# Kernel tuning notes

Hardware: AMD Instinct MI355X
Metric: run time of the kernel (lower is better)

The kernel has to match this reference:

```python
import jax, jax.numpy as jnp
import numpy as np

B, L, SIZE, ATT, LIN = 8, 2048, 1024, 1024, 4096
EPS = 1e-5


def layer_norm(x, g, b):
    m = x.mean(-1, keepdims=True)
    v = ((x - m) ** 2).mean(-1, keepdims=True)
    return (x - m) * jax.lax.rsqrt(v + EPS) * g + b


def time_shift(x):
    # ZeroPad2d((0,0,1,-1)): prepend a zero timestep, drop the last one
    return jnp.pad(x, ((0, 0), (1, 0), (0, 0)))[:, :-1]


def wkv(time_decay, time_first, k, v):
    """RWKV-v4 WKV linear-attention recurrence (numerically stable, log-space max tracking).
    k, v: (B, L, D). Returns (B, L, D)."""
    w = -jnp.exp(time_decay)  # (D,) per-channel decay (negative)
    u = time_first            # (D,) bonus for current token

    def step(carry, kv):
        p, q, o = carry  # numerator, denominator, running max exponent: (B, D)
        kt, vt = kv      # (B, D)
        no = jnp.maximum(o, u + kt)
        A = jnp.exp(o - no)
        Bc = jnp.exp(u + kt - no)
        out = (A * p + Bc * vt) / (A * q + Bc)
        no2 = jnp.maximum(o + w, kt)
        A2 = jnp.exp(o + w - no2)
        B2 = jnp.exp(kt - no2)
        return (A2 * p + B2 * vt, A2 * q + B2, no2), out

    Bn, Ln, D = k.shape
    init = (jnp.zeros((Bn, D), k.dtype), jnp.zeros((Bn, D), k.dtype),
            jnp.full((Bn, D), -1e38, k.dtype))
    _, out = jax.lax.scan(step, init, (jnp.moveaxis(k, 1, 0), jnp.moveaxis(v, 1, 0)))
    return jnp.moveaxis(out, 0, 1)


def setup_inputs() -> dict:
    key = jax.random.key(0)
    ks = jax.random.split(key, 20)
    n = lambda i, shape, s=1.0: jax.random.normal(ks[i], shape, jnp.float32) * s
    u = lambda i, shape: jax.random.uniform(ks[i], shape, jnp.float32)
    return {
        "x": n(0, (B, L, SIZE)),
        "ln_att_g": jnp.ones((SIZE,), jnp.float32), "ln_att_b": jnp.zeros((SIZE,), jnp.float32),
        "ln_ffn_g": jnp.ones((SIZE,), jnp.float32), "ln_ffn_b": jnp.zeros((SIZE,), jnp.float32),
        "att_time_decay": n(1, (ATT,), 0.5), "att_time_first": n(2, (ATT,), 0.5),
        "att_mix_k": u(3, (SIZE,)), "att_mix_v": u(4, (SIZE,)), "att_mix_r": u(5, (SIZE,)),
        "att_wk": n(6, (SIZE, ATT), 0.02), "att_wv": n(7, (SIZE, ATT), 0.02),
        "att_wr": n(8, (SIZE, ATT), 0.02), "att_wo": n(9, (ATT, SIZE), 0.02),
        "ffn_mix_k": u(10, (SIZE,)), "ffn_mix_r": u(11, (SIZE,)),
        "ffn_wk": n(12, (SIZE, LIN), 0.02), "ffn_wv": n(13, (LIN, SIZE), 0.02),
        "ffn_wr": n(14, (SIZE, SIZE), 0.02),
    }


def reference(x, ln_att_g, ln_att_b, ln_ffn_g, ln_ffn_b,
              att_time_decay, att_time_first, att_mix_k, att_mix_v, att_mix_r,
              att_wk, att_wv, att_wr, att_wo,
              ffn_mix_k, ffn_mix_r, ffn_wk, ffn_wv, ffn_wr):
    # --- time-mixing (WKV attention) branch ---
    h = layer_norm(x, ln_att_g, ln_att_b)
    sx = time_shift(h)
    k = (h * att_mix_k + sx * (1.0 - att_mix_k)) @ att_wk
    v = (h * att_mix_v + sx * (1.0 - att_mix_v)) @ att_wv
    r = jax.nn.sigmoid((h * att_mix_r + sx * (1.0 - att_mix_r)) @ att_wr)
    att = (r * wkv(att_time_decay, att_time_first, k, v)) @ att_wo
    x = x + att  # dropout rate 0.0 (eval)
    # --- channel-mixing (FFN) branch ---
    h = layer_norm(x, ln_ffn_g, ln_ffn_b)
    sx = time_shift(h)
    kf = jnp.square(jax.nn.relu((h * ffn_mix_k + sx * (1.0 - ffn_mix_k)) @ ffn_wk))
    rf = jax.nn.sigmoid((h * ffn_mix_r + sx * (1.0 - ffn_mix_r)) @ ffn_wr)
    return x + rf * (kf @ ffn_wv)
```

## Files before the change

### kernel.cpp

```cpp
#include <hip/hip_runtime.h>
#include <cstdint>
#include <cstddef>

#define BB   8
#define LLEN 2048
#define DSZ  1024
#define FFN  4096
#define MROWS (BB*LLEN)
#define EPSLN 1e-5f
#define WKV_C 32
#define WKV_S (LLEN/WKV_C)
#define WKV_STATES (BB*WKV_C*DSZ)

typedef __bf16 bh8 __attribute__((ext_vector_type(8)));
typedef float  f32x4 __attribute__((ext_vector_type(4)));

__device__ __forceinline__ unsigned short f32_to_bf16(float f) {
  unsigned int u = __float_as_uint(f);
  u += 0x7FFFu + ((u >> 16) & 1u);
  return (unsigned short)(u >> 16);
}
__device__ __forceinline__ float bf16_to_f32(unsigned short u) {
  return __uint_as_float(((unsigned int)u) << 16);
}
__device__ __forceinline__ float bf16_lo(unsigned int u) {
  return __uint_as_float(u << 16);
}
__device__ __forceinline__ float bf16_hi(unsigned int u) {
  return __uint_as_float(u & 0xFFFF0000u);
}
__device__ __forceinline__ unsigned int pack_bf16(float lo, float hi) {
  return (unsigned int)f32_to_bf16(lo) | ((unsigned int)f32_to_bf16(hi) << 16);
}

__device__ __forceinline__ void load_lds16(const void* g, void* l) {
  __builtin_amdgcn_global_load_lds((const __attribute__((address_space(1))) void*)g,
                                   (__attribute__((address_space(3))) void*)l, 16, 0, 0);
}

#define RAW_BAR() asm volatile("s_barrier" ::: "memory")
#define WAIT_VM6() asm volatile("s_waitcnt vmcnt(6)" ::: "memory")
#define WAIT_VM0() asm volatile("s_waitcnt vmcnt(0)" ::: "memory")

__global__ __launch_bounds__(256) void transpose_bf16(const float* __restrict__ W,
                                                      unsigned short* __restrict__ Wt,
                                                      int K, int N) {
  __shared__ float tile[32][33];
  int n0 = blockIdx.x * 32, k0 = blockIdx.y * 32;
  int tx = threadIdx.x, ty = threadIdx.y;
#pragma unroll
  for (int j = 0; j < 32; j += 8)
    tile[ty + j][tx] = W[(size_t)(k0 + ty + j) * N + n0 + tx];
  __syncthreads();
#pragma unroll
  for (int j = 0; j < 32; j += 8)
    Wt[(size_t)(n0 + ty + j) * K + k0 + tx] = f32_to_bf16(tile[tx][ty + j]);
}

__global__ __launch_bounds__(256) void lnmix_att(const float* __restrict__ x,
                                                 const float* __restrict__ g,
                                                 const float* __restrict__ bb,
                                                 const float* __restrict__ mk,
                                                 const float* __restrict__ mv,
                                                 const float* __restrict__ mr,
                                                 unsigned short* __restrict__ xk,
                                                 unsigned short* __restrict__ xv,
                                                 unsigned short* __restrict__ xr) {
  int row = blockIdx.x;
  int t = row & (LLEN - 1);
  int tid = threadIdx.x;
  float4 vc = ((const float4*)(x + (size_t)row * DSZ))[tid];
  float4 vp = make_float4(0.f, 0.f, 0.f, 0.f);
  if (t > 0) vp = ((const float4*)(x + (size_t)(row - 1) * DSZ))[tid];
  float sc = vc.x + vc.y + vc.z + vc.w;
  float qc = vc.x * vc.x + vc.y * vc.y + vc.z * vc.z + vc.w * vc.w;
  float sp = vp.x + vp.y + vp.z + vp.w;
  float qp = vp.x * vp.x + vp.y * vp.y + vp.z * vp.z + vp.w * vp.w;
#pragma unroll
  for (int off = 32; off; off >>= 1) {
    sc += __shfl_down(sc, off); qc += __shfl_down(qc, off);
    sp += __shfl_down(sp, off); qp += __shfl_down(qp, off);
  }
  __shared__ float red[16];
  int lane = tid & 63, w = tid >> 6;
  if (lane == 0) { red[w] = sc; red[4 + w] = qc; red[8 + w] = sp; red[12 + w] = qp; }
  __syncthreads();
  if (tid < 4) red[tid * 4] = red[tid * 4] + red[tid * 4 + 1] + red[tid * 4 + 2] + red[tid * 4 + 3];
  __syncthreads();
  const float invD = 1.f / DSZ;
  float mc = red[0] * invD, rc = rsqrtf(red[4] * invD - mc * mc + EPSLN);
  float mp = red[8] * invD, rp = rsqrtf(red[12] * invD - mp * mp + EPSLN);
  float4 G = ((const float4*)g)[tid], Bv = ((const float4*)bb)[tid];
  float c[4] = { vc.x, vc.y, vc.z, vc.w };
  float p[4] = { vp.x, vp.y, vp.z, vp.w };
  float Ga[4] = { G.x, G.y, G.z, G.w };
  float Ba[4] = { Bv.x, Bv.y, Bv.z, Bv.w };
  float4 K = ((const float4*)mk)[tid];
  float4 V = ((const float4*)mv)[tid];
  float4 R = ((const float4*)mr)[tid];
  float Ka[4] = { K.x, K.y, K.z, K.w };
  float Va[4] = { V.x, V.y, V.z, V.w };
  float Ra[4] = { R.x, R.y, R.z, R.w };
  ushort4 ok, ov, orr;
  unsigned short* okp = &ok.x; unsigned short* ovp = &ov.x; unsigned short* orp = &orr.x;
#pragma unroll
  for (int e = 0; e < 4; ++e) {
    float hc = (c[e] - mc) * rc * Ga[e] + Ba[e];
    float hp = (t > 0) ? (p[e] - mp) * rp * Ga[e] + Ba[e] : 0.f;
    okp[e] = f32_to_bf16(hc * Ka[e] + hp * (1.f - Ka[e]));
    ovp[e] = f32_to_bf16(hc * Va[e] + hp * (1.f - Va[e]));
    orp[e] = f32_to_bf16(hc * Ra[e] + hp * (1.f - Ra[e]));
  }
  size_t e4 = (size_t)row * DSZ + tid * 4;
  *(ushort4*)(xk + e4) = ok;
  *(ushort4*)(xv + e4) = ov;
  *(ushort4*)(xr + e4) = orr;
}

__global__ __launch_bounds__(256) void lnmix_ffn(const float* __restrict__ x,
                                                 const float* __restrict__ g,
                                                 const float* __restrict__ bb,
                                                 const float* __restrict__ mk,
                                                 const float* __restrict__ mr,
                                                 unsigned short* __restrict__ xk,
                                                 unsigned short* __restrict__ xr) {
  int row = blockIdx.x;
  int t = row & (LLEN - 1);
  int tid = threadIdx.x;
  float4 vc = ((const float4*)(x + (size_t)row * DSZ))[tid];
  float4 vp = make_float4(0.f, 0.f, 0.f, 0.f);
  if (t > 0) vp = ((const float4*)(x + (size_t)(row - 1) * DSZ))[tid];
  float sc = vc.x + vc.y + vc.z + vc.w;
  float qc = vc.x * vc.x + vc.y * vc.y + vc.z * vc.z + vc.w * vc.w;
  float sp = vp.x + vp.y + vp.z + vp.w;
  float qp = vp.x * vp.x + vp.y * vp.y + vp.z * vp.z + vp.w * vp.w;
#pragma unroll
  for (int off = 32; off; off >>= 1) {
    sc += __shfl_down(sc, off); qc += __shfl_down(qc, off);
    sp += __shfl_down(sp, off); qp += __shfl_down(qp, off);
  }
  __shared__ float red[16];
  int lane = tid & 63, w = tid >> 6;
  if (lane == 0) { red[w] = sc; red[4 + w] = qc; red[8 + w] = sp; red[12 + w] = qp; }
  __syncthreads();
  if (tid < 4) red[tid * 4] = red[tid * 4] + red[tid * 4 + 1] + red[tid * 4 + 2] + red[tid * 4 + 3];
  __syncthreads();
  const float invD = 1.f / DSZ;
  float mc = red[0] * invD, rc = rsqrtf(red[4] * invD - mc * mc + EPSLN);
  float mp = red[8] * invD, rp = rsqrtf(red[12] * invD - mp * mp + EPSLN);
  float4 G = ((const float4*)g)[tid], Bv = ((const float4*)bb)[tid];
  float c[4] = { vc.x, vc.y, vc.z, vc.w };
  float p[4] = { vp.x, vp.y, vp.z, vp.w };
  float Ga[4] = { G.x, G.y, G.z, G.w };
  float Ba[4] = { Bv.x, Bv.y, Bv.z, Bv.w };
  float4 K = ((const float4*)mk)[tid];
  float4 R = ((const float4*)mr)[tid];
  float Ka[4] = { K.x, K.y, K.z, K.w };
  float Ra[4] = { R.x, R.y, R.z, R.w };
  ushort4 ok, orr;
  unsigned short* okp = &ok.x; unsigned short* orp = &orr.x;
#pragma unroll
  for (int e = 0; e < 4; ++e) {
    float hc = (c[e] - mc) * rc * Ga[e] + Ba[e];
    float hp = (t > 0) ? (p[e] - mp) * rp * Ga[e] + Ba[e] : 0.f;
    okp[e] = f32_to_bf16(hc * Ka[e] + hp * (1.f - Ka[e]));
    orp[e] = f32_to_bf16(hc * Ra[e] + hp * (1.f - Ra[e]));
  }
  size_t e4 = (size_t)row * DSZ + tid * 4;
  *(ushort4*)(xk + e4) = ok;
  *(ushort4*)(xr + e4) = orr;
}

__global__ __launch_bounds__(256) void wkv_pass1(const unsigned int* __restrict__ kk2,
                                                 const unsigned int* __restrict__ vv2,
                                                 const float* __restrict__ td,
                                                 float* __restrict__ sP,
                                                 float* __restrict__ sQ,
                                                 float* __restrict__ sO) {
  int gid = blockIdx.x * 256 + threadIdx.x;
  int d2 = gid & 511;
  int bc = gid >> 9;
  int c  = bc & (WKV_C - 1);
  int b  = bc >> 5;
  int d0 = d2 * 2;
  float w0 = -expf(td[d0]), w1 = -expf(td[d0 + 1]);
  size_t base = ((size_t)b * LLEN + (size_t)c * WKV_S) * 512 + d2;
  float p0 = 0.f, q0 = 0.f, o0 = -1e38f;
  float p1 = 0.f, q1 = 0.f, o1 = -1e38f;
  unsigned int kc = kk2[base], vc = vv2[base];
  unsigned int kA = 0, vA = 0, kB = 0, vB = 0;
  if (WKV_S > 1) { kA = kk2[base + 512]; vA = vv2[base + 512]; }
  for (int t = 0; t < WKV_S; ++t) {
    if (t + 2 < WKV_S) {
      size_t nxt = base + (size_t)(t + 2) * 512;
      kB = kk2[nxt]; vB = vv2[nxt];
    } else { kB = 0; vB = 0; }
    {
      float kt = bf16_lo(kc), vt = bf16_lo(vc);
      float ow = o0 + w0;
      float no2 = fmaxf(ow, kt);
      float A2 = expf(ow - no2), B2 = expf(kt - no2);
      p0 = A2 * p0 + B2 * vt; q0 = A2 * q0 + B2; o0 = no2;
    }
    {
      float kt = bf16_hi(kc), vt = bf16_hi(vc);
      float ow = o1 + w1;
      float no2 = fmaxf(ow, kt);
      float A2 = expf(ow - no2), B2 = expf(kt - no2);
      p1 = A2 * p1 + B2 * vt; q1 = A2 * q1 + B2; o1 = no2;
    }
    kc = kA; vc = vA; kA = kB; vA = vB;
  }
  int sidx = (bc << 10) + d0;
  sP[sidx] = p0; sP[sidx + 1] = p1;
  sQ[sidx] = q0; sQ[sidx + 1] = q1;
  sO[sidx] = o0; sO[sidx + 1] = o1;
}

__global__ __launch_bounds__(256) void wkv_combine(const float* __restrict__ sP,
                                                   const float* __restrict__ sQ,
                                                   const float* __restrict__ sO,
                                                   const float* __restrict__ td,
                                                   float* __restrict__ pP,
                                                   float* __restrict__ pQ,
                                                   float* __restrict__ pO) {
  int gid = blockIdx.x * 256 + threadIdx.x;
  int d = gid & (DSZ - 1);
  int b = gid >> 10;
  float w = -expf(td[d]);
  float Sw = (float)WKV_S * w;
  float p = 0.f, q = 0.f, o = -1e38f;
  for (int c = 0; c < WKV_C; ++c) {
    size_t idx = (((size_t)b * WKV_C + c) << 10) + d;
    pP[idx] = p; pQ[idx] = q; pO[idx] = o;
    float lp = sP[idx], lq = sQ[idx], lo = sO[idx];
    float oin = o + Sw;
    float no  = fmaxf(oin, lo);
    float Ai  = expf(oin - no);
    float Al  = expf(lo - no);
    p = Ai * p + Al * lp;
    q = Ai * q + Al * lq;
    o = no;
  }
}

__global__ __launch_bounds__(256) void wkv_pass3(const unsigned int* __restrict__ kk2,
                                                 const unsigned int* __restrict__ vv2,
                                                 const unsigned int* __restrict__ rr2,
                                                 const float* __restrict__ td,
                                                 const float* __restrict__ tf,
                                                 const float* __restrict__ pP,
                                                 const float* __restrict__ pQ,
                                                 const float* __restrict__ pO,
                                                 unsigned int* __restrict__ rw2) {
  int gid = blockIdx.x * 256 + threadIdx.x;
  int d2 = gid & 511;
  int bc = gid >> 9;
  int c  = bc & (WKV_C - 1);
  int b  = bc >> 5;
  int d0 = d2 * 2;
  float w0 = -expf(td[d0]), w1 = -expf(td[d0 + 1]);
  float u0 = tf[d0], u1 = tf[d0 + 1];
  int sidx = (bc << 10) + d0;
  float p0 = pP[sidx], q0 = pQ[sidx], o0 = pO[sidx];
  float p1 = pP[sidx + 1], q1 = pQ[sidx + 1], o1 = pO[sidx + 1];
  size_t base = ((size_t)b * LLEN + (size_t)c * WKV_S) * 512 + d2;
  unsigned int kc = kk2[base], vc = vv2[base], rc = rr2[base];
  unsigned int kA = 0, vA = 0, rA = 0, kB = 0, vB = 0, rB = 0;
  if (WKV_S > 1) { kA = kk2[base + 512]; vA = vv2[base + 512]; rA = rr2[base + 512]; }
  for (int t = 0; t < WKV_S; ++t) {
    if (t + 2 < WKV_S) {
      size_t nxt = base + (size_t)(t + 2) * 512;
      kB = kk2[nxt]; vB = vv2[nxt]; rB = rr2[nxt];
    } else { kB = 0; vB = 0; rB = 0; }
    float out0, out1;
    {
      float kt = bf16_lo(kc), vt = bf16_lo(vc);
      float uk = u0 + kt;
      float no = fmaxf(o0, uk);
      float A  = expf(o0 - no), Bc = expf(uk - no);
      out0 = (A * p0 + Bc * vt) / (A * q0 + Bc);
      float ow = o0 + w0;
      float no2 = fmaxf(ow, kt);
      float A2 = expf(ow - no2), B2 = expf(kt - no2);
      p0 = A2 * p0 + B2 * vt; q0 = A2 * q0 + B2; o0 = no2;
    }
    {
      float kt = bf16_hi(kc), vt = bf16_hi(vc);
      float uk = u1 + kt;
      float no = fmaxf(o1, uk);
      float A  = expf(o1 - no), Bc = expf(uk - no);
      out1 = (A * p1 + Bc * vt) / (A * q1 + Bc);
      float ow = o1 + w1;
      float no2 = fmaxf(ow, kt);
      float A2 = expf(ow - no2), B2 = expf(kt - no2);
      p1 = A2 * p1 + B2 * vt; q1 = A2 * q1 + B2; o1 = no2;
    }
    rw2[base + (size_t)t * 512] = pack_bf16(bf16_lo(rc) * out0, bf16_hi(rc) * out1);
    kc = kA; vc = vA; rc = rA; kA = kB; vA = vB; rA = rB;
  }
}


__device__ __forceinline__ void stage_half(const unsigned short* __restrict__ gsrc,
                                           int Kd, unsigned char* lds_base,
                                           int lane, int wid) {
  int gcol = (((lane & 7) ^ (lane >> 3)) << 3);
  int grow = lane >> 3;
#pragma unroll
  for (int j = 0; j < 2; ++j) {
    int win = wid * 2 + j;
    const unsigned short* src = gsrc + (size_t)(win * 8 + grow) * Kd + gcol;
    load_lds16(src, lds_base + win * 1024 + lane * 16);
  }
}

template <int EPI>
__global__ __launch_bounds__(512, 2) void gemm256(const unsigned short* __restrict__ A,
                                                  const unsigned short* __restrict__ Bt,
                                                  float* __restrict__ C,
                                                  unsigned short* __restrict__ Cbf,
                                                  const float* __restrict__ aux1,
                                                  const unsigned short* __restrict__ aux2b,
                                                  int M, int N, int K) {
  extern __shared__ unsigned char sm[];
  unsigned char* smA = sm;
  unsigned char* smB = sm + 65536;

  const int tid  = threadIdx.x;
  const int lane = tid & 63;
  const int wid  = tid >> 6;
  const int wr   = wid >> 2;
  const int wc   = wid & 3;

  int nwg = gridDim.x;
  int gx  = N >> 8;
  int wg  = blockIdx.x;
  int swzid = ((nwg & 7) == 0) ? ((wg & 7) * (nwg >> 3) + (wg >> 3)) : wg;
  int bn = swzid % gx, bm = swzid / gx;

  const unsigned short* Ab = A  + (size_t)bm * 256 * K;
  const unsigned short* Bb = Bt + (size_t)bn * 256 * K;

  const int nk = K >> 6;

  const int r15 = lane & 15;
  const int sw0 = ((((lane >> 4)    ) ^ (lane & 7)) << 4);
  const int sw1 = (((4 | (lane >> 4)) ^ (lane & 7)) << 4);
  const int aRow = wr * 16384 + r15 * 128;
  const int bRow = wc * 8192  + r15 * 128;

  f32x4 acc[8][4];
#pragma unroll
  for (int i = 0; i < 8; ++i)
#pragma unroll
    for (int j = 0; j < 4; ++j)
#pragma unroll
      for (int e = 0; e < 4; ++e) acc[i][j][e] = 0.f;

  stage_half(Ab,                 K, smA,                 lane, wid);
  stage_half(Ab + (size_t)128*K, K, smA + 16384,         lane, wid);
  stage_half(Bb,                 K, smB,                 lane, wid);
  stage_half(Bb + (size_t)128*K, K, smB + 16384,         lane, wid);
  if (nk > 1) {
    stage_half(Bb + 64,                 K, smB + 32768,         lane, wid);
    stage_half(Ab + 64,                 K, smA + 32768,         lane, wid);
    stage_half(Ab + (size_t)128*K + 64, K, smA + 32768 + 16384, lane, wid);
    WAIT_VM6();
  } else {
    WAIT_VM0();
  }
  RAW_BAR();

  bh8 a03[4][2], a47[4][2], b01[2][2], b23[2][2];

  for (int t = 0; t < nk; ++t) {
    const int buf  = (t & 1) * 32768;
    const int bufn = buf ^ 32768;
    const int kb1  = (t + 1) << 6;
    const int kb2  = (t + 2) << 6;

#pragma unroll
    for (int mi = 0; mi < 4; ++mi) {
      a03[mi][0] = *(const bh8*)(smA + buf + aRow + mi * 2048 + sw0);
      a03[mi][1] = *(const bh8*)(smA + buf + aRow + mi * 2048 + sw1);
    }
#pragma unroll
    for (int nj = 0; nj < 2; ++nj) {
      b01[nj][0] = *(const bh8*)(smB + buf + bRow + nj * 2048 + sw0);
      b01[nj][1] = *(const bh8*)(smB + buf + bRow + nj * 2048 + sw1);
    }
    if (t + 1 < nk)
      stage_half(Bb + (size_t)128*K + kb1, K, smB + bufn + 16384, lane, wid);
    RAW_BAR();
    __builtin_amdgcn_s_setprio(1);
#pragma unroll
    for (int mi = 0; mi < 4; ++mi)
#pragma unroll
      for (int nj = 0; nj < 2; ++nj) {
        acc[mi][nj] = __builtin_amdgcn_mfma_f32_16x16x32_bf16(a03[mi][0], b01[nj][0], acc[mi][nj], 0, 0, 0);
        acc[mi][nj] = __builtin_amdgcn_mfma_f32_16x16x32_bf16(a03[mi][1], b01[nj][1], acc[mi][nj], 0, 0, 0);
      }
    __builtin_amdgcn_s_setprio(0);
    RAW_BAR();

#pragma unroll
    for (int nj = 0; nj < 2; ++nj) {
      b23[nj][0] = *(const bh8*)(smB + buf + bRow + (nj + 2) * 2048 + sw0);
      b23[nj][1] = *(const bh8*)(smB + buf + bRow + (nj + 2) * 2048 + sw1);
    }
    RAW_BAR();
    __builtin_amdgcn_s_setprio(1);
#pragma unroll
    for (int mi = 0; mi < 4; ++mi)
#pragma unroll
      for (int nj = 0; nj < 2; ++nj) {
        acc[mi][nj + 2] = __builtin_amdgcn_mfma_f32_16x16x32_bf16(a03[mi][0], b23[nj][0], acc[mi][nj + 2], 0, 0, 0);
        acc[mi][nj + 2] = __builtin_amdgcn_mfma_f32_16x16x32_bf16(a03[mi][1], b23[nj][1], acc[mi][nj + 2], 0, 0, 0);
      }
    __builtin_amdgcn_s_setprio(0);
    RAW_BAR();

#pragma unroll
    for (int mi = 0; mi < 4; ++mi) {
      a47[mi][0] = *(const bh8*)(smA + buf + aRow + (mi + 4) * 2048 + sw0);
      a47[mi][1] = *(const bh8*)(smA + buf + aRow + (mi + 4) * 2048 + sw1);
    }
    if (t + 2 < nk) stage_half(Bb + kb2, K, smB + buf, lane, wid);
    RAW_BAR();
    __builtin_amdgcn_s_setprio(1);
#pragma unroll
    for (int mi = 0; mi < 4; ++mi)
#pragma unroll
      for (int nj = 0; nj < 2; ++nj) {
        acc[mi + 4][nj] = __builtin_amdgcn_mfma_f32_16x16x32_bf16(a47[mi][0], b01[nj][0], acc[mi + 4][nj], 0, 0, 0);
        acc[mi + 4][nj] = __builtin_amdgcn_mfma_f32_16x16x32_bf16(a47[mi][1], b01[nj][1], acc[mi + 4][nj], 0, 0, 0);
      }
    __builtin_amdgcn_s_setprio(0);
    RAW_BAR();

    if (t + 2 < nk) {
      stage_half(Ab + kb2,                 K, smA + buf,         lane, wid);
      stage_half(Ab + (size_t)128*K + kb2, K, smA + buf + 16384, lane, wid);
    }
    RAW_BAR();
    __builtin_amdgcn_s_setprio(1);
#pragma unroll
    for (int mi = 0; mi < 4; ++mi)
#pragma unroll
      for (int nj = 0; nj < 2; ++nj) {
        acc[mi + 4][nj + 2] = __builtin_amdgcn_mfma_f32_16x16x32_bf16(a47[mi][0], b23[nj][0], acc[mi + 4][nj + 2], 0, 0, 0);
        acc[mi + 4][nj + 2] = __builtin_amdgcn_mfma_f32_16x16x32_bf16(a47[mi][1], b23[nj][1], acc[mi + 4][nj + 2], 0, 0, 0);
      }
    __builtin_amdgcn_s_setprio(0);
    if (t + 2 < nk) { WAIT_VM6(); } else { WAIT_VM0(); }
    RAW_BAR();
  }

  const int r4 = (lane >> 4) * 4, cn = lane & 15;
#pragma unroll
  for (int mi = 0; mi < 8; ++mi) {
#pragma unroll
    for (int nj = 0; nj < 4; ++nj) {
      int col = bn * 256 + wc * 64 + nj * 16 + cn;
#pragma unroll
      for (int e = 0; e < 4; ++e) {
        int row = bm * 256 + wr * 128 + mi * 16 + r4 + e;
        size_t idx = (size_t)row * N + col;
        float val = acc[mi][nj][e];
        if (EPI == 0) {
          Cbf[idx] = f32_to_bf16(val);
        } else if (EPI == 1) {
          Cbf[idx] = f32_to_bf16(1.f / (1.f + expf(-val)));
        } else if (EPI == 2) {
          C[idx] = aux1[idx] + val;
        } else if (EPI == 3) {
          float tt = val > 0.f ? val : 0.f;
          Cbf[idx] = f32_to_bf16(tt * tt);
        } else {
          C[idx] = aux1[idx] + bf16_to_f32(aux2b[idx]) * val;
        }
      }
    }
  }
}

extern "C" void kernel_launch(void* const* d_in, const int* in_sizes, int n_in,
                              void* d_out, int out_size, void* d_ws, size_t ws_size,
                              hipStream_t stream) {
  const float* x        = (const float*)d_in[0];
  const float* ln_att_g = (const float*)d_in[1];
  const float* ln_att_b = (const float*)d_in[2];
  const float* ln_ffn_g = (const float*)d_in[3];
  const float* ln_ffn_b = (const float*)d_in[4];
  const float* td       = (const float*)d_in[5];
  const float* tf       = (const float*)d_in[6];
  const float* amk      = (const float*)d_in[7];
  const float* amv      = (const float*)d_in[8];
  const float* amr      = (const float*)d_in[9];
  const float* att_wk   = (const float*)d_in[10];
  const float* att_wv   = (const float*)d_in[11];
  const float* att_wr   = (const float*)d_in[12];
  const float* att_wo   = (const float*)d_in[13];
  const float* fmk      = (const float*)d_in[14];
  const float* fmr      = (const float*)d_in[15];
  const float* ffn_wk   = (const float*)d_in[16];
  const float* ffn_wv   = (const float*)d_in[17];
  const float* ffn_wr   = (const float*)d_in[18];
  float* out = (float*)d_out;
  (void)in_sizes; (void)n_in; (void)out_size;

  const size_t WBYTES  = 4 * ((size_t)DSZ * DSZ * 2)
                       + (size_t)FFN * DSZ * 2
                       + (size_t)DSZ * FFN * 2
                       + (size_t)DSZ * DSZ * 2;
  const size_t BUF     = (size_t)MROWS * DSZ * 2;
  const size_t NEEDED  = WBYTES + 4 * BUF + 2 * BUF;
  if (ws_size < NEEDED) return;

  char* ws = (char*)d_ws;
  size_t off = 0;
  auto take = [&](size_t bytes) { char* p = ws + off; off += (bytes + 255) & ~(size_t)255; return p; };

  unsigned short* wkT  = (unsigned short*)take((size_t)DSZ * DSZ * 2);
  unsigned short* wvT  = (unsigned short*)take((size_t)DSZ * DSZ * 2);
  unsigned short* wrT  = (unsigned short*)take((size_t)DSZ * DSZ * 2);
  unsigned short* woT  = (unsigned short*)take((size_t)DSZ * DSZ * 2);
  unsigned short* fwkT = (unsigned short*)take((size_t)FFN * DSZ * 2);
  unsigned short* fwvT = (unsigned short*)take((size_t)DSZ * FFN * 2);
  unsigned short* fwrT = (unsigned short*)take((size_t)DSZ * DSZ * 2);
  unsigned short* bufA = (unsigned short*)take(BUF);
  unsigned short* bufB = (unsigned short*)take(BUF);
  unsigned short* bufC = (unsigned short*)take(BUF);
  unsigned short* bufD = (unsigned short*)take(BUF);
  char*           eReg = take(2 * BUF);
  unsigned short* kf = bufC;

  float* sP = (float*)eReg;
  float* sQ = sP + WKV_STATES;
  float* sO = sQ + WKV_STATES;
  float* pP = sO + WKV_STATES;
  float* pQ = pP + WKV_STATES;
  float* pO = pQ + WKV_STATES;

  dim3 tb(32, 8);
  transpose_bf16<<<dim3(DSZ / 32, DSZ / 32), tb, 0, stream>>>(att_wk, wkT, DSZ, DSZ);
  transpose_bf16<<<dim3(DSZ / 32, DSZ / 32), tb, 0, stream>>>(att_wv, wvT, DSZ, DSZ);
  transpose_bf16<<<dim3(DSZ / 32, DSZ / 32), tb, 0, stream>>>(att_wr, wrT, DSZ, DSZ);
  transpose_bf16<<<dim3(DSZ / 32, DSZ / 32), tb, 0, stream>>>(att_wo, woT, DSZ, DSZ);
  transpose_bf16<<<dim3(FFN / 32, DSZ / 32), tb, 0, stream>>>(ffn_wk, fwkT, DSZ, FFN);
  transpose_bf16<<<dim3(DSZ / 32, FFN / 32), tb, 0, stream>>>(ffn_wv, fwvT, FFN, DSZ);
  transpose_bf16<<<dim3(DSZ / 32, DSZ / 32), tb, 0, stream>>>(ffn_wr, fwrT, DSZ, DSZ);

  const int LDSB = 131072;
  const int G1   = (MROWS / 256) * (DSZ / 256);
  const int G2   = (MROWS / 256) * (FFN / 256);

  lnmix_att<<<MROWS, 256, 0, stream>>>(x, ln_att_g, ln_att_b, amk, amv, amr, bufA, bufB, bufC);
  gemm256<0><<<G1, 512, LDSB, stream>>>(bufA, wkT, nullptr, bufD, nullptr, nullptr, MROWS, DSZ, DSZ);
  gemm256<0><<<G1, 512, LDSB, stream>>>(bufB, wvT, nullptr, bufA, nullptr, nullptr, MROWS, DSZ, DSZ);
  gemm256<1><<<G1, 512, LDSB, stream>>>(bufC, wrT, nullptr, bufB, nullptr, nullptr, MROWS, DSZ, DSZ);
  wkv_pass1<<<(WKV_STATES / 2) / 256, 256, 0, stream>>>((const unsigned int*)bufD, (const unsigned int*)bufA, td, sP, sQ, sO);
  wkv_combine<<<(BB * DSZ) / 256, 256, 0, stream>>>(sP, sQ, sO, td, pP, pQ, pO);
  wkv_pass3<<<(WKV_STATES / 2) / 256, 256, 0, stream>>>((const unsigned int*)bufD, (const unsigned int*)bufA, (const unsigned int*)bufB, td, tf, pP, pQ, pO, (unsigned int*)bufC);
  gemm256<2><<<G1, 512, LDSB, stream>>>(bufC, woT, out, nullptr, x, nullptr, MROWS, DSZ, DSZ);

  lnmix_ffn<<<MROWS, 256, 0, stream>>>(out, ln_ffn_g, ln_ffn_b, fmk, fmr, bufA, bufB);
  gemm256<3><<<G2, 512, LDSB, stream>>>(bufA, fwkT, nullptr, kf, nullptr, nullptr, MROWS, FFN, DSZ);
  gemm256<1><<<G1, 512, LDSB, stream>>>(bufB, fwrT, nullptr, bufA, nullptr, nullptr, MROWS, DSZ, DSZ);
  gemm256<4><<<G1, 512, LDSB, stream>>>(kf, fwvT, out, nullptr, out, bufA, MROWS, DSZ, FFN);
}
```

Before: 685.5 us.

## Replace 256x256 pipelined GEMM with simpler 128x256 tile, BK=32 double-buffered kernel

Swaps the hand-scheduled 256x256 GEMM (BK=64, staged quarter-loads, setprio, raw barriers) for a 128x256 tile kernel with BK=32, one-ahead double buffering and a single __syncthreads per k-step. LDS use drops from 128 KB to 48 KB and launch bounds allow 4 blocks per CU, aiming for more occupancy and simpler latency hiding. In exchange, each block does less reuse per byte loaded, runs fewer MFMAs between barriers, and loses the fine-grained interleaving of loads and compute.

```diff
diff --git a/kernel.cpp b/kernel.cpp
--- a/kernel.cpp
+++ b/kernel.cpp
@@ -37,10 +37,6 @@
   __builtin_amdgcn_global_load_lds((const __attribute__((address_space(1))) void*)g,
                                    (__attribute__((address_space(3))) void*)l, 16, 0, 0);
 }
-
-#define RAW_BAR() asm volatile("s_barrier" ::: "memory")
-#define WAIT_VM6() asm volatile("s_waitcnt vmcnt(6)" ::: "memory")
-#define WAIT_VM0() asm volatile("s_waitcnt vmcnt(0)" ::: "memory")
 
 __global__ __launch_bounds__(256) void transpose_bf16(const float* __restrict__ W,
                                                       unsigned short* __restrict__ Wt,
@@ -301,31 +297,17 @@
   }
 }
 
-
-__device__ __forceinline__ void stage_half(const unsigned short* __restrict__ gsrc,
-                                           int Kd, unsigned char* lds_base,
-                                           int lane, int wid) {
-  int gcol = (((lane & 7) ^ (lane >> 3)) << 3);
-  int grow = lane >> 3;
-#pragma unroll
-  for (int j = 0; j < 2; ++j) {
-    int win = wid * 2 + j;
-    const unsigned short* src = gsrc + (size_t)(win * 8 + grow) * Kd + gcol;
-    load_lds16(src, lds_base + win * 1024 + lane * 16);
-  }
-}
-
 template <int EPI>
-__global__ __launch_bounds__(512, 2) void gemm256(const unsigned short* __restrict__ A,
-                                                  const unsigned short* __restrict__ Bt,
-                                                  float* __restrict__ C,
-                                                  unsigned short* __restrict__ Cbf,
-                                                  const float* __restrict__ aux1,
-                                                  const unsigned short* __restrict__ aux2b,
-                                                  int M, int N, int K) {
+__global__ __launch_bounds__(512, 4) void gemmTile(const unsigned short* __restrict__ A,
+                                                   const unsigned short* __restrict__ Bt,
+                                                   float* __restrict__ C,
+                                                   unsigned short* __restrict__ Cbf,
+                                                   const float* __restrict__ aux1,
+                                                   const unsigned short* __restrict__ aux2b,
+                                                   int M, int N, int K) {
   extern __shared__ unsigned char sm[];
   unsigned char* smA = sm;
-  unsigned char* smB = sm + 65536;
+  unsigned char* smB = sm + 16384;
 
   const int tid  = threadIdx.x;
   const int lane = tid & 63;
@@ -339,133 +321,70 @@
   int swzid = ((nwg & 7) == 0) ? ((wg & 7) * (nwg >> 3) + (wg >> 3)) : wg;
   int bn = swzid % gx, bm = swzid / gx;
 
-  const unsigned short* Ab = A  + (size_t)bm * 256 * K;
+  const unsigned short* Ab = A  + (size_t)bm * 128 * K;
   const unsigned short* Bb = Bt + (size_t)bn * 256 * K;
-
-  const int nk = K >> 6;
-
-  const int r15 = lane & 15;
-  const int sw0 = ((((lane >> 4)    ) ^ (lane & 7)) << 4);
-  const int sw1 = (((4 | (lane >> 4)) ^ (lane & 7)) << 4);
-  const int aRow = wr * 16384 + r15 * 128;
-  const int bRow = wc * 8192  + r15 * 128;
-
-  f32x4 acc[8][4];
-#pragma unroll
-  for (int i = 0; i < 8; ++i)
+  const int nk = K >> 5;
+
+  const int srow = tid >> 2;
+  const int aCol = (((tid & 3) ^ (srow & 3)) << 3);
+  const unsigned short* pA  = Ab + (size_t)srow * K + aCol;
+  const unsigned short* pB0 = Bb + (size_t)srow * K + aCol;
+  const unsigned short* pB1 = Bb + (size_t)(128 + srow) * K + aCol;
+  const int ldsA  = tid * 16;
+  const int ldsB0 = tid * 16;
+  const int ldsB1 = tid * 16 + 8192;
+
+  const int r16 = lane & 15;
+  const int swz = (((lane >> 4) ^ (r16 & 3)) << 4);
+  const int aOff = (wr * 64 + r16) * 64 + swz;
+  const int bOff = (wc * 64 + r16) * 64 + swz;
+
+  f32x4 acc[4][4];
+#pragma unroll
+  for (int i = 0; i < 4; ++i)
 #pragma unroll
     for (int j = 0; j < 4; ++j)
 #pragma unroll
       for (int e = 0; e < 4; ++e) acc[i][j][e] = 0.f;
 
-  stage_half(Ab,                 K, smA,                 lane, wid);
-  stage_half(Ab + (size_t)128*K, K, smA + 16384,         lane, wid);
-  stage_half(Bb,                 K, smB,                 lane, wid);
-  stage_half(Bb + (size_t)128*K, K, smB + 16384,         lane, wid);
-  if (nk > 1) {
-    stage_half(Bb + 64,                 K, smB + 32768,         lane, wid);
-    stage_half(Ab + 64,                 K, smA + 32768,         lane, wid);
-    stage_half(Ab + (size_t)128*K + 64, K, smA + 32768 + 16384, lane, wid);
-    WAIT_VM6();
-  } else {
-    WAIT_VM0();
-  }
-  RAW_BAR();
-
-  bh8 a03[4][2], a47[4][2], b01[2][2], b23[2][2];
+  load_lds16(pA,  smA + ldsA);
+  load_lds16(pB0, smB + ldsB0);
+  load_lds16(pB1, smB + ldsB1);
+  __syncthreads();
 
   for (int t = 0; t < nk; ++t) {
-    const int buf  = (t & 1) * 32768;
-    const int bufn = buf ^ 32768;
-    const int kb1  = (t + 1) << 6;
-    const int kb2  = (t + 2) << 6;
-
-#pragma unroll
-    for (int mi = 0; mi < 4; ++mi) {
-      a03[mi][0] = *(const bh8*)(smA + buf + aRow + mi * 2048 + sw0);
-      a03[mi][1] = *(const bh8*)(smA + buf + aRow + mi * 2048 + sw1);
-    }
-#pragma unroll
-    for (int nj = 0; nj < 2; ++nj) {
-      b01[nj][0] = *(const bh8*)(smB + buf + bRow + nj * 2048 + sw0);
-      b01[nj][1] = *(const bh8*)(smB + buf + bRow + nj * 2048 + sw1);
-    }
-    if (t + 1 < nk)
-      stage_half(Bb + (size_t)128*K + kb1, K, smB + bufn + 16384, lane, wid);
-    RAW_BAR();
-    __builtin_amdgcn_s_setprio(1);
+    const int buf  = t & 1;
+    const int bufn = buf ^ 1;
+    if (t + 1 < nk) {
+      int ko = (t + 1) << 5;
+      load_lds16(pA + ko,  smA + bufn * 8192  + ldsA);
+      load_lds16(pB0 + ko, smB + bufn * 16384 + ldsB0);
+      load_lds16(pB1 + ko, smB + bufn * 16384 + ldsB1);
+    }
+    bh8 a[4], b[4];
 #pragma unroll
     for (int mi = 0; mi < 4; ++mi)
-#pragma unroll
-      for (int nj = 0; nj < 2; ++nj) {
-        acc[mi][nj] = __builtin_amdgcn_mfma_f32_16x16x32_bf16(a03[mi][0], b01[nj][0], acc[mi][nj], 0, 0, 0);
-        acc[mi][nj] = __builtin_amdgcn_mfma_f32_16x16x32_bf16(a03[mi][1], b01[nj][1], acc[mi][nj], 0, 0, 0);
-      }
-    __builtin_amdgcn_s_setprio(0);
-    RAW_BAR();
-
-#pragma unroll
-    for (int nj = 0; nj < 2; ++nj) {
-      b23[nj][0] = *(const bh8*)(smB + buf + bRow + (nj + 2) * 2048 + sw0);
-      b23[nj][1] = *(const bh8*)(smB + buf + bRow + (nj + 2) * 2048 + sw1);
-    }
-    RAW_BAR();
-    __builtin_amdgcn_s_setprio(1);
+      a[mi] = *(const bh8*)(smA + buf * 8192 + aOff + mi * 1024);
+#pragma unroll
+    for (int nj = 0; nj < 4; ++nj)
+      b[nj] = *(const bh8*)(smB + buf * 16384 + bOff + nj * 1024);
 #pragma unroll
     for (int mi = 0; mi < 4; ++mi)
 #pragma unroll
-      for (int nj = 0; nj < 2; ++nj) {
-        acc[mi][nj + 2] = __builtin_amdgcn_mfma_f32_16x16x32_bf16(a03[mi][0], b23[nj][0], acc[mi][nj + 2], 0, 0, 0);
-        acc[mi][nj + 2] = __builtin_amdgcn_mfma_f32_16x16x32_bf16(a03[mi][1], b23[nj][1], acc[mi][nj + 2], 0, 0, 0);
-      }
-    __builtin_amdgcn_s_setprio(0);
-    RAW_BAR();
-
-#pragma unroll
-    for (int mi = 0; mi < 4; ++mi) {
-      a47[mi][0] = *(const bh8*)(smA + buf + aRow + (mi + 4) * 2048 + sw0);
-      a47[mi][1] = *(const bh8*)(smA + buf + aRow + (mi + 4) * 2048 + sw1);
-    }
-    if (t + 2 < nk) stage_half(Bb + kb2, K, smB + buf, lane, wid);
-    RAW_BAR();
-    __builtin_amdgcn_s_setprio(1);
-#pragma unroll
-    for (int mi = 0; mi < 4; ++mi)
-#pragma unroll
-      for (int nj = 0; nj < 2; ++nj) {
-        acc[mi + 4][nj] = __builtin_amdgcn_mfma_f32_16x16x32_bf16(a47[mi][0], b01[nj][0], acc[mi + 4][nj], 0, 0, 0);
-        acc[mi + 4][nj] = __builtin_amdgcn_mfma_f32_16x16x32_bf16(a47[mi][1], b01[nj][1], acc[mi + 4][nj], 0, 0, 0);
-      }
-    __builtin_amdgcn_s_setprio(0);
-    RAW_BAR();
-
-    if (t + 2 < nk) {
-      stage_half(Ab + kb2,                 K, smA + buf,         lane, wid);
-      stage_half(Ab + (size_t)128*K + kb2, K, smA + buf + 16384, lane, wid);
-    }
-    RAW_BAR();
-    __builtin_amdgcn_s_setprio(1);
-#pragma unroll
-    for (int mi = 0; mi < 4; ++mi)
-#pragma unroll
-      for (int nj = 0; nj < 2; ++nj) {
-        acc[mi + 4][nj + 2] = __builtin_amdgcn_mfma_f32_16x16x32_bf16(a47[mi][0], b23[nj][0], acc[mi + 4][nj + 2], 0, 0, 0);
-        acc[mi + 4][nj + 2] = __builtin_amdgcn_mfma_f32_16x16x32_bf16(a47[mi][1], b23[nj][1], acc[mi + 4][nj + 2], 0, 0, 0);
-      }
-    __builtin_amdgcn_s_setprio(0);
-    if (t + 2 < nk) { WAIT_VM6(); } else { WAIT_VM0(); }
-    RAW_BAR();
+      for (int nj = 0; nj < 4; ++nj)
+        acc[mi][nj] = __builtin_amdgcn_mfma_f32_16x16x32_bf16(a[mi], b[nj], acc[mi][nj], 0, 0, 0);
+    __syncthreads();
   }
 
   const int r4 = (lane >> 4) * 4, cn = lane & 15;
 #pragma unroll
-  for (int mi = 0; mi < 8; ++mi) {
+  for (int mi = 0; mi < 4; ++mi) {
 #pragma unroll
     for (int nj = 0; nj < 4; ++nj) {
       int col = bn * 256 + wc * 64 + nj * 16 + cn;
 #pragma unroll
       for (int e = 0; e < 4; ++e) {
-        int row = bm * 256 + wr * 128 + mi * 16 + r4 + e;
+        int row = bm * 128 + wr * 64 + mi * 16 + r4 + e;
         size_t idx = (size_t)row * N + col;
         float val = acc[mi][nj][e];
         if (EPI == 0) {
@@ -552,21 +471,21 @@
   transpose_bf16<<<dim3(DSZ / 32, FFN / 32), tb, 0, stream>>>(ffn_wv, fwvT, FFN, DSZ);
   transpose_bf16<<<dim3(DSZ / 32, DSZ / 32), tb, 0, stream>>>(ffn_wr, fwrT, DSZ, DSZ);
 
-  const int LDSB = 131072;
-  const int G1   = (MROWS / 256) * (DSZ / 256);
-  const int G2   = (MROWS / 256) * (FFN / 256);
+  const int LDSB = 49152;
+  const int G1   = (MROWS / 128) * (DSZ / 256);
+  const int G2   = (MROWS / 128) * (FFN / 256);
 
   lnmix_att<<<MROWS, 256, 0, stream>>>(x, ln_att_g, ln_att_b, amk, amv, amr, bufA, bufB, bufC);
-  gemm256<0><<<G1, 512, LDSB, stream>>>(bufA, wkT, nullptr, bufD, nullptr, nullptr, MROWS, DSZ, DSZ);
-  gemm256<0><<<G1, 512, LDSB, stream>>>(bufB, wvT, nullptr, bufA, nullptr, nullptr, MROWS, DSZ, DSZ);
-  gemm256<1><<<G1, 512, LDSB, stream>>>(bufC, wrT, nullptr, bufB, nullptr, nullptr, MROWS, DSZ, DSZ);
+  gemmTile<0><<<G1, 512, LDSB, stream>>>(bufA, wkT, nullptr, bufD, nullptr, nullptr, MROWS, DSZ, DSZ);
+  gemmTile<0><<<G1, 512, LDSB, stream>>>(bufB, wvT, nullptr, bufA, nullptr, nullptr, MROWS, DSZ, DSZ);
+  gemmTile<1><<<G1, 512, LDSB, stream>>>(bufC, wrT, nullptr, bufB, nullptr, nullptr, MROWS, DSZ, DSZ);
   wkv_pass1<<<(WKV_STATES / 2) / 256, 256, 0, stream>>>((const unsigned int*)bufD, (const unsigned int*)bufA, td, sP, sQ, sO);
   wkv_combine<<<(BB * DSZ) / 256, 256, 0, stream>>>(sP, sQ, sO, td, pP, pQ, pO);
   wkv_pass3<<<(WKV_STATES / 2) / 256, 256, 0, stream>>>((const unsigned int*)bufD, (const unsigned int*)bufA, (const unsigned int*)bufB, td, tf, pP, pQ, pO, (unsigned int*)bufC);
-  gemm256<2><<<G1, 512, LDSB, stream>>>(bufC, woT, out, nullptr, x, nullptr, MROWS, DSZ, DSZ);
+  gemmTile<2><<<G1, 512, LDSB, stream>>>(bufC, woT, out, nullptr, x, nullptr, MROWS, DSZ, DSZ);
 
   lnmix_ffn<<<MROWS, 256, 0, stream>>>(out, ln_ffn_g, ln_ffn_b, fmk, fmr, bufA, bufB);
-  gemm256<3><<<G2, 512, LDSB, stream>>>(bufA, fwkT, nullptr, kf, nullptr, nullptr, MROWS, FFN, DSZ);
-  gemm256<1><<<G1, 512, LDSB, stream>>>(bufB, fwrT, nullptr, bufA, nullptr, nullptr, MROWS, DSZ, DSZ);
-  gemm256<4><<<G1, 512, LDSB, stream>>>(kf, fwvT, out, nullptr, out, bufA, MROWS, DSZ, FFN);
-}
+  gemmTile<3><<<G2, 512, LDSB, stream>>>(bufA, fwkT, nullptr, kf, nullptr, nullptr, MROWS, FFN, DSZ);
+  gemmTile<1><<<G1, 512, LDSB, stream>>>(bufB, fwrT, nullptr, bufA, nullptr, nullptr, MROWS, DSZ, DSZ);
+  gemmTile<4><<<G1, 512, LDSB, stream>>>(kf, fwvT, out, nullptr, out, bufA, MROWS, DSZ, FFN);
+}
```

Result: slower. 738.3 us (+7.7%).
